# Performance work log

Hardware: AMD Instinct MI355X
Metric: run time of the kernel (lower is better)

The kernel has to match this reference:

```python
import jax, jax.numpy as jnp
import numpy as np

NUM_LANDMARKS = 256
PINV_ITERS = 6


def iterative_inv(K):
    # Newton-Schulz iterative pseudo-inverse (Nystromformer), K: [B, m, m]
    I = jnp.eye(K.shape[-1], dtype=K.dtype)
    V = K.swapaxes(-1, -2) / (jnp.max(jnp.sum(K, axis=-2)) * jnp.max(jnp.sum(K, axis=-1)))
    for _ in range(PINV_ITERS):
        KV = K @ V
        V = 0.25 * V @ (13.0 * I - KV @ (15.0 * I - KV @ (7.0 * I - KV)))
    return V


def nystrom_attention_matrix(q, k, m):
    # q, k: [B, N, d] -> approximate softmax(q k^T / sqrt(d)) of shape [B, N, N]
    B, N, d = q.shape
    scale = 1.0 / jnp.sqrt(jnp.asarray(d, q.dtype))
    L = N // m
    q_l = q.reshape(B, m, L, d).mean(axis=2)  # landmark queries [B, m, d]
    k_l = k.reshape(B, m, L, d).mean(axis=2)  # landmark keys    [B, m, d]
    k1 = jax.nn.softmax(jnp.einsum('bnd,bmd->bnm', q, k_l) * scale, axis=-1)   # [B, N, m]
    k2 = jax.nn.softmax(jnp.einsum('bld,bmd->blm', q_l, k_l) * scale, axis=-1) # [B, m, m]
    k3 = jax.nn.softmax(jnp.einsum('bmd,bnd->bmn', q_l, k) * scale, axis=-1)   # [B, m, N]
    return (k1 @ iterative_inv(k2)) @ k3  # [B, N, N]


def setup_inputs() -> dict:
    key = jax.random.key(0)
    ks = jax.random.split(key, 8)
    B, C, T, W, H = 2, 64, 4, 32, 32
    d = C // 8
    scale = 0.05  # keep q.k scores in a sane softmax range
    return {
        'x': jax.random.normal(ks[0], (B, C, T, W, H), dtype=jnp.float32),
        'wq': jax.random.normal(ks[1], (d, C), dtype=jnp.float32) * scale,
        'bq': jax.random.normal(ks[2], (d,), dtype=jnp.float32) * scale,
        'wk': jax.random.normal(ks[3], (d, C), dtype=jnp.float32) * scale,
        'bk': jax.random.normal(ks[4], (d,), dtype=jnp.float32) * scale,
        'wv': jax.random.normal(ks[5], (C, C), dtype=jnp.float32) * scale,
        'bv': jax.random.normal(ks[6], (C,), dtype=jnp.float32) * scale,
        'gamma': jax.random.normal(ks[7], (1,), dtype=jnp.float32),
    }


def reference(x, wq, bq, wk, bk, wv, bv, gamma):
    B, C, T, W, H = x.shape
    N = T * W * H
    xf = x.reshape(B, C, N)
    # 1x1x1 Conv3d == per-token linear over channels
    q = jnp.einsum('oc,bcn->bno', wq, xf) + bq            # [B, N, C//8]
    k = jnp.einsum('oc,bcn->bno', wk, xf) + bk            # [B, N, C//8]
    v = jnp.einsum('oc,bcn->bon', wv, xf) + bv[None, :, None]  # [B, C, N]
    attn = nystrom_attention_matrix(q, k, NUM_LANDMARKS)  # [B, N, N]
    # out = bmm(value, attn^T): out[b,c,i] = sum_j v[b,c,j] * attn[b,i,j]
    out = jnp.einsum('bcj,bij->bci', v, attn).reshape(B, C, T, W, H)
    out = gamma[0] * out + x
    return out, attn
```

## Files before the change

### kernel.cpp

```cpp
#include <hip/hip_runtime.h>
#include <hip/hip_bf16.h>
#include <math.h>

#define NB 2
#define NC 64
#define ND 8
#define NN 4096
#define NM 256
#define NL 16
#define SCALE 0.35355339059327373f
#define A_ROOT 4.1303956f
#define B_COEF (-2.8696044f)
#define C_COEF 3.1474086f

typedef __attribute__((ext_vector_type(4))) float f32x4;
typedef __attribute__((ext_vector_type(8))) short bf16x8;

__device__ inline ushort f2bf(float f) {
  __hip_bfloat16 h = __float2bfloat16(f);
  return *reinterpret_cast<ushort*>(&h);
}
__device__ inline float bf2f(ushort u) {
  return __uint_as_float(((unsigned int)u) << 16);
}

__device__ inline void gl_lds16(const void* g, void* l) {
  __builtin_amdgcn_global_load_lds(
      (const __attribute__((address_space(1))) unsigned int*)g,
      (__attribute__((address_space(3))) unsigned int*)l, 16, 0, 0);
}

__global__ __launch_bounds__(256) void qkv2_kernel(
    const float* __restrict__ x,
    const float* __restrict__ wq, const float* __restrict__ bq,
    const float* __restrict__ wk, const float* __restrict__ bk,
    const float* __restrict__ wv, const float* __restrict__ bv,
    float* __restrict__ q, float* __restrict__ k, float* __restrict__ v) {
  __shared__ float ws[NC];
  int o = blockIdx.x;
  int b = blockIdx.z;
  int n0 = blockIdx.y * 1024;
  int t = threadIdx.x;
  const float* wrow;
  float bias;
  if (o < ND)            { wrow = wq + (size_t)o * NC;            bias = bq[o]; }
  else if (o < 2 * ND)   { wrow = wk + (size_t)(o - ND) * NC;     bias = bk[o - ND]; }
  else                   { wrow = wv + (size_t)(o - 2 * ND) * NC; bias = bv[o - 2 * ND]; }
  if (t < NC) ws[t] = wrow[t];
  __syncthreads();
  int n = n0 + t * 4;
  float4 acc = {bias, bias, bias, bias};
  #pragma unroll
  for (int c = 0; c < NC; ++c) {
    float wc = ws[c];
    float4 xv = *(const float4*)(x + ((size_t)b * NC + c) * NN + n);
    acc.x += wc * xv.x; acc.y += wc * xv.y; acc.z += wc * xv.z; acc.w += wc * xv.w;
  }
  if (o < ND) {
    float* qp = q + ((size_t)b * NN + n) * ND + o;
    qp[0] = acc.x; qp[8] = acc.y; qp[16] = acc.z; qp[24] = acc.w;
  } else if (o < 2 * ND) {
    float* kp = k + ((size_t)b * NN + n) * ND + (o - ND);
    kp[0] = acc.x; kp[8] = acc.y; kp[16] = acc.z; kp[24] = acc.w;
  } else {
    *(float4*)(v + ((size_t)b * NC + (o - 2 * ND)) * NN + n) = acc;
  }
}

__global__ void landmark_kernel(const float* __restrict__ q, const float* __restrict__ k,
                                float* __restrict__ ql, float* __restrict__ kl) {
  int idx = blockIdx.x * 256 + threadIdx.x;
  int b = idx / (NM * ND), r = idx % (NM * ND), i = r / ND, o = r % ND;
  float sq = 0.f, sk = 0.f;
  for (int l = 0; l < NL; ++l) {
    size_t base = ((size_t)b * NN + i * NL + l) * ND + o;
    sq += q[base]; sk += k[base];
  }
  ql[idx] = sq * (1.0f / NL);
  kl[idx] = sk * (1.0f / NL);
}

__global__ __launch_bounds__(256) void scores_softmax_m_bf16(
    const float* __restrict__ Q, int R, const float* __restrict__ KL,
    ushort* __restrict__ out) {
  __shared__ float skl[NM][9];
  int b = blockIdx.y;
  int t = threadIdx.x;
  for (int i = t; i < NM * ND; i += 256) skl[i >> 3][i & 7] = KL[(size_t)b * NM * ND + i];
  __syncthreads();
  int wave = t >> 6, lane = t & 63;
  int r = blockIdx.x * 4 + wave;
  const float* qrow = Q + ((size_t)b * R + r) * ND;
  float qr[ND];
  #pragma unroll
  for (int dd = 0; dd < ND; ++dd) qr[dd] = qrow[dd];
  float sc[4];
  float lmax = -1e30f;
  #pragma unroll
  for (int s = 0; s < 4; ++s) {
    int j = lane + 64 * s;
    float a = 0.f;
    #pragma unroll
    for (int dd = 0; dd < ND; ++dd) a += qr[dd] * skl[j][dd];
    sc[s] = a * SCALE;
    lmax = fmaxf(lmax, sc[s]);
  }
  for (int off = 32; off; off >>= 1) lmax = fmaxf(lmax, __shfl_xor(lmax, off));
  float lsum = 0.f;
  #pragma unroll
  for (int s = 0; s < 4; ++s) { sc[s] = expf(sc[s] - lmax); lsum += sc[s]; }
  for (int off = 32; off; off >>= 1) lsum += __shfl_xor(lsum, off);
  float inv = 1.0f / lsum;
  #pragma unroll
  for (int s = 0; s < 4; ++s)
    out[((size_t)b * R + r) * NM + lane + 64 * s] = f2bf(sc[s] * inv);
}

__global__ __launch_bounds__(256) void scores_softmax_m_f32(
    const float* __restrict__ Q, int R, const float* __restrict__ KL,
    float* __restrict__ out) {
  __shared__ float skl[NM][9];
  int b = blockIdx.y;
  int t = threadIdx.x;
  for (int i = t; i < NM * ND; i += 256) skl[i >> 3][i & 7] = KL[(size_t)b * NM * ND + i];
  __syncthreads();
  int wave = t >> 6, lane = t & 63;
  int r = blockIdx.x * 4 + wave;
  const float* qrow = Q + ((size_t)b * R + r) * ND;
  float qr[ND];
  #pragma unroll
  for (int dd = 0; dd < ND; ++dd) qr[dd] = qrow[dd];
  float sc[4];
  float lmax = -1e30f;
  #pragma unroll
  for (int s = 0; s < 4; ++s) {
    int j = lane + 64 * s;
    float a = 0.f;
    #pragma unroll
    for (int dd = 0; dd < ND; ++dd) a += qr[dd] * skl[j][dd];
    sc[s] = a * SCALE;
    lmax = fmaxf(lmax, sc[s]);
  }
  for (int off = 32; off; off >>= 1) lmax = fmaxf(lmax, __shfl_xor(lmax, off));
  float lsum = 0.f;
  #pragma unroll
  for (int s = 0; s < 4; ++s) { sc[s] = expf(sc[s] - lmax); lsum += sc[s]; }
  for (int off = 32; off; off >>= 1) lsum += __shfl_xor(lsum, off);
  float inv = 1.0f / lsum;
  #pragma unroll
  for (int s = 0; s < 4; ++s) out[((size_t)b * R + r) * NM + lane + 64 * s] = sc[s] * inv;
}

__global__ __launch_bounds__(256) void scores_softmax_n(
    const float* __restrict__ QL, const float* __restrict__ Kt,
    float* __restrict__ out) {
  __shared__ float wred[4], wsum[4];
  int b = blockIdx.y, i = blockIdx.x;
  int t = threadIdx.x;
  float qr[ND];
  #pragma unroll
  for (int dd = 0; dd < ND; ++dd) qr[dd] = QL[((size_t)b * NM + i) * ND + dd];
  float sc[16];
  float lmax = -1e30f;
  #pragma unroll
  for (int s = 0; s < 16; ++s) {
    int n = t + 256 * s;
    const float* kp = Kt + ((size_t)b * NN + n) * ND;
    float a = 0.f;
    #pragma unroll
    for (int dd = 0; dd < ND; ++dd) a += qr[dd] * kp[dd];
    sc[s] = a * SCALE;
    lmax = fmaxf(lmax, sc[s]);
  }
  for (int off = 32; off; off >>= 1) lmax = fmaxf(lmax, __shfl_xor(lmax, off));
  if ((t & 63) == 0) wred[t >> 6] = lmax;
  __syncthreads();
  lmax = fmaxf(fmaxf(wred[0], wred[1]), fmaxf(wred[2], wred[3]));
  float lsum = 0.f;
  #pragma unroll
  for (int s = 0; s < 16; ++s) { sc[s] = expf(sc[s] - lmax); lsum += sc[s]; }
  for (int off = 32; off; off >>= 1) lsum += __shfl_xor(lsum, off);
  if ((t & 63) == 0) wsum[t >> 6] = lsum;
  __syncthreads();
  lsum = wsum[0] + wsum[1] + wsum[2] + wsum[3];
  float inv = 1.0f / lsum;
  #pragma unroll
  for (int s = 0; s < 16; ++s) out[((size_t)b * NM + i) * NN + t + 256 * s] = sc[s] * inv;
}

__global__ __launch_bounds__(256) void denom_kernel(const float* __restrict__ k2,
                                                    float* __restrict__ denw) {
  __shared__ float red[256];
  int b = blockIdx.x;
  int t = threadIdx.x;
  float cs = 0.f;
  for (int i = 0; i < NM; ++i) cs += k2[((size_t)b * NM + i) * NM + t];
  red[t] = cs;
  __syncthreads();
  for (int off = 128; off; off >>= 1) {
    if (t < off) red[t] = fmaxf(red[t], red[t + off]);
    __syncthreads();
  }
  if (t == 0) denw[b] = red[0];
}

__global__ void vinit_kernel(const float* __restrict__ k2, const float* __restrict__ denw,
                             float* __restrict__ V) {
  int idx = blockIdx.x * 256 + threadIdx.x;
  int b = idx / (NM * NM), r = idx % (NM * NM), i = r / NM, j = r % NM;
  float dval = 1.0f / fmaxf(denw[0], denw[1]);
  V[idx] = k2[((size_t)b * NM + j) * NM + i] * dval;
}

#define NS_SMEM 70144

__device__ __forceinline__ void pad_work(
    int p, const float* __restrict__ k3, ushort* __restrict__ k3t,
    const float* __restrict__ vw, float* __restrict__ kvw, char* smem, int t) {
  if (p < 2048) {
    typedef float TRow[33];
    TRow* tile = (TRow*)smem;
    int n0 = (p & 127) * 32, m0 = ((p >> 7) & 7) * 32, b = p >> 10;
    int rr = t >> 3, c4 = (t & 7) * 4;
    float4 v = *(const float4*)(k3 + ((size_t)b * NM + m0 + rr) * NN + n0 + c4);
    tile[c4][rr] = v.x; tile[c4 + 1][rr] = v.y; tile[c4 + 2][rr] = v.z; tile[c4 + 3][rr] = v.w;
    __syncthreads();
    ushort4 u;
    u.x = f2bf(tile[rr][c4]);     u.y = f2bf(tile[rr][c4 + 1]);
    u.z = f2bf(tile[rr][c4 + 2]); u.w = f2bf(tile[rr][c4 + 3]);
    *(ushort4*)(k3t + ((size_t)b * NN + n0 + rr) * NM + m0 + c4) = u;
  } else {
    typedef float KVRow[33];
    KVRow* Ks = (KVRow*)smem;
    KVRow* Vs = (KVRow*)(smem + 64 * 33 * 4);
    int p2 = p - 2048;
    int bp = (p2 & 3) * 64;
    int jsl = (p2 >> 2) & 31;
    int b = p2 >> 7;
    int j0base = jsl * (NN / 32);
    int tx = t & 15, ty = t >> 4;
    int lrow = t >> 2, ljc = (t & 3) * 8;
    float acc[4][4] = {};
    for (int j0 = j0base; j0 < j0base + NN / 32; j0 += 32) {
      float4 a0 = *(const float4*)(k3 + ((size_t)b * NM + bp + lrow) * NN + j0 + ljc);
      float4 a1 = *(const float4*)(k3 + ((size_t)b * NM + bp + lrow) * NN + j0 + ljc + 4);
      float4 v0 = *(const float4*)(vw + ((size_t)b * NC + lrow) * NN + j0 + ljc);
      float4 v1 = *(const float4*)(vw + ((size_t)b * NC + lrow) * NN + j0 + ljc + 4);
      Ks[lrow][ljc + 0] = a0.x; Ks[lrow][ljc + 1] = a0.y; Ks[lrow][ljc + 2] = a0.z; Ks[lrow][ljc + 3] = a0.w;
      Ks[lrow][ljc + 4] = a1.x; Ks[lrow][ljc + 5] = a1.y; Ks[lrow][ljc + 6] = a1.z; Ks[lrow][ljc + 7] = a1.w;
      Vs[lrow][ljc + 0] = v0.x; Vs[lrow][ljc + 1] = v0.y; Vs[lrow][ljc + 2] = v0.z; Vs[lrow][ljc + 3] = v0.w;
      Vs[lrow][ljc + 4] = v1.x; Vs[lrow][ljc + 5] = v1.y; Vs[lrow][ljc + 6] = v1.z; Vs[lrow][ljc + 7] = v1.w;
      __syncthreads();
      #pragma unroll
      for (int kk = 0; kk < 32; ++kk) {
        float av_[4], bv_[4];
        #pragma unroll
        for (int i = 0; i < 4; ++i) av_[i] = Ks[(ty << 2) + i][kk];
        #pragma unroll
        for (int j = 0; j < 4; ++j) bv_[j] = Vs[(tx << 2) + j][kk];
        #pragma unroll
        for (int i = 0; i < 4; ++i)
          #pragma unroll
          for (int j = 0; j < 4; ++j) acc[i][j] += av_[i] * bv_[j];
      }
      __syncthreads();
    }
    #pragma unroll
    for (int i = 0; i < 4; ++i)
      #pragma unroll
      for (int j = 0; j < 4; ++j)
        atomicAdd(&kvw[((size_t)b * NM + bp + (ty << 2) + i) * NC + (tx << 2) + j], acc[i][j]);
  }
}

__device__ __forceinline__ void ns_tile(
    const float* __restrict__ A, const float* __restrict__ B,
    const float* __restrict__ B2, float* __restrict__ O,
    float s_a, float s_ab, size_t bo, int bi, int bj, char* smem, int t) {
  typedef float ARow[260];
  typedef float BRow[36];
  ARow* As = (ARow*)smem;
  BRow* Bs = (BRow*)(smem + 33280);
  #pragma unroll
  for (int q = 0; q < 8; ++q) {
    int s = q * 256 + t;
    int ar = s >> 6, ac = (s & 63) * 4;
    *(float4*)&As[ar][ac] = *(const float4*)(A + bo + (size_t)(bi + ar) * NM + ac);
    int bk = s >> 3, bc = (s & 7) * 4;
    if (B2 == nullptr) {
      *(float4*)&Bs[bk][bc] = *(const float4*)(B + bo + (size_t)bk * NM + bj + bc);
    } else {
      float4 v = *(const float4*)(B + bo + (size_t)bk * NM + bj + bc);
      float4 z = *(const float4*)(B2 + bo + (size_t)bk * NM + bj + bc);
      float4 rr;
      rr.x = v.x + B_COEF * z.x; rr.y = v.y + B_COEF * z.y;
      rr.z = v.z + B_COEF * z.z; rr.w = v.w + B_COEF * z.w;
      int d = bk - bj - bc;
      if (d >= 0 && d < 4) ((float*)&rr)[d] += C_COEF;
      *(float4*)&Bs[bk][bc] = rr;
    }
  }
  __syncthreads();
  int tx = t & 15, ty = t >> 4;
  float acc[2][2] = {};
  #pragma unroll 8
  for (int kk = 0; kk < NM; ++kk) {
    float a0 = As[ty * 2][kk], a1 = As[ty * 2 + 1][kk];
    float b0 = Bs[kk][tx * 2], b1 = Bs[kk][tx * 2 + 1];
    acc[0][0] += a0 * b0; acc[0][1] += a0 * b1;
    acc[1][0] += a1 * b0; acc[1][1] += a1 * b1;
  }
  #pragma unroll
  for (int i = 0; i < 2; ++i)
    #pragma unroll
    for (int j = 0; j < 2; ++j) {
      size_t o = bo + (size_t)(bi + ty * 2 + i) * NM + bj + tx * 2 + j;
      float r = s_ab * acc[i][j];
      if (s_a != 0.0f) r += s_a * A[o];
      O[o] = r;
    }
}

__global__ __launch_bounds__(256) void ns_z_kernel(
    const float* __restrict__ k2, const float* __restrict__ V, float* __restrict__ Z,
    const float* __restrict__ k3, ushort* __restrict__ k3t,
    const float* __restrict__ vw, float* __restrict__ kvw, int padBase) {
  __shared__ char smem[NS_SMEM];
  int blk = blockIdx.x, t = threadIdx.x;
  if (blk < NB * 64) {
    int b = blk >> 6, tile = blk & 63;
    int bi = (tile >> 3) * 32, bj = (tile & 7) * 32;
    ns_tile(k2, V, nullptr, Z, 0.f, 1.f, (size_t)b * NM * NM, bi, bj, smem, t);
  } else {
    pad_work(padBase + blk - NB * 64, k3, k3t, vw, kvw, smem, t);
  }
}

__global__ __launch_bounds__(256) void ns_uz2_kernel(
    const float* __restrict__ V, const float* __restrict__ Z,
    float* __restrict__ U, float* __restrict__ Z2,
    const float* __restrict__ k3, ushort* __restrict__ k3t,
    const float* __restrict__ vw, float* __restrict__ kvw, int padBase) {
  __shared__ char smem[NS_SMEM];
  int blk = blockIdx.x, t = threadIdx.x;
  if (blk < NB * 64) {
    int b = blk >> 6, tile = blk & 63;
    int bi = (tile >> 3) * 32, bj = (tile & 7) * 32;
    ns_tile(V, Z, nullptr, U, -A_ROOT, 1.f, (size_t)b * NM * NM, bi, bj, smem, t);
  } else if (blk < 2 * NB * 64) {
    int r = blk - NB * 64;
    int b = r >> 6, tile = r & 63;
    int bi = (tile >> 3) * 32, bj = (tile & 7) * 32;
    ns_tile(Z, Z, nullptr, Z2, 0.f, 1.f, (size_t)b * NM * NM, bi, bj, smem, t);
  } else {
    pad_work(padBase + blk - 2 * NB * 64, k3, k3t, vw, kvw, smem, t);
  }
}

__global__ __launch_bounds__(256) void ns_v_kernel(
    const float* __restrict__ U, const float* __restrict__ Z2,
    const float* __restrict__ Z, float* __restrict__ Vout,
    const float* __restrict__ k3, ushort* __restrict__ k3t,
    const float* __restrict__ vw, float* __restrict__ kvw, int padBase) {
  __shared__ char smem[NS_SMEM];
  int blk = blockIdx.x, t = threadIdx.x;
  if (blk < NB * 64) {
    int b = blk >> 6, tile = blk & 63;
    int bi = (tile >> 3) * 32, bj = (tile & 7) * 32;
    ns_tile(U, Z2, Z, Vout, 0.f, -0.25f, (size_t)b * NM * NM, bi, bj, smem, t);
  } else {
    pad_work(padBase + blk - NB * 64, k3, k3t, vw, kvw, smem, t);
  }
}

__global__ __launch_bounds__(256) void cvt_vinv_kernel(const float* __restrict__ Va,
                                                       ushort* __restrict__ Vt) {
  int b = blockIdx.z;
  int n0 = blockIdx.x * 32, m0 = blockIdx.y * 32;
  __shared__ float tile[32][33];
  int t = threadIdx.x;
  int r = t >> 3, c4 = (t & 7) * 4;
  float4 v = *(const float4*)(Va + ((size_t)b * NM + m0 + r) * NM + n0 + c4);
  tile[c4][r] = v.x; tile[c4 + 1][r] = v.y; tile[c4 + 2][r] = v.z; tile[c4 + 3][r] = v.w;
  __syncthreads();
  ushort4 u;
  u.x = f2bf(tile[r][c4]);     u.y = f2bf(tile[r][c4 + 1]);
  u.z = f2bf(tile[r][c4 + 2]); u.w = f2bf(tile[r][c4 + 3]);
  *(ushort4*)(Vt + ((size_t)b * NM + n0 + r) * NM + m0 + c4) = u;
}

__global__ __launch_bounds__(256) void gemm_a_mfma(
    const ushort* __restrict__ k1bf, const ushort* __restrict__ Vt,
    ushort* __restrict__ Abf) {
  int b = blockIdx.z;
  int bi = blockIdx.y * 128, bj = blockIdx.x * 128;
  __shared__ ushort As[128 * 64];
  __shared__ ushort Bs[128 * 64];
  int t = threadIdx.x;
  int wave = t >> 6, lane = t & 63;
  int wr = wave >> 1, wc = wave & 1;
  const ushort* Ab = k1bf + (size_t)b * NN * NM;
  const ushort* Bb = Vt + (size_t)b * NM * NM;
  f32x4 acc[4][4] = {};
  for (int k0 = 0; k0 < NM; k0 += 64) {
    #pragma unroll
    for (int q = 0; q < 4; ++q) {
      int s = q * 256 + t;
      int r = s >> 3, c = s & 7;
      int cs = (c ^ (r & 7)) << 3;
      gl_lds16(Ab + (size_t)(bi + r) * NM + k0 + cs, As + (size_t)s * 8);
      gl_lds16(Bb + (size_t)(bj + r) * NM + k0 + cs, Bs + (size_t)s * 8);
    }
    __syncthreads();
    #pragma unroll
    for (int kk = 0; kk < 2; ++kk) {
      int koff = kk * 64 + (lane >> 4) * 16;
      bf16x8 af[4], bfv[4];
      #pragma unroll
      for (int mi = 0; mi < 4; ++mi) {
        int row = wr * 64 + mi * 16 + (lane & 15);
        af[mi] = *(const bf16x8*)((const char*)As + row * 128 + (koff ^ ((row & 7) << 4)));
      }
      #pragma unroll
      for (int nj = 0; nj < 4; ++nj) {
        int row = wc * 64 + nj * 16 + (lane & 15);
        bfv[nj] = *(const bf16x8*)((const char*)Bs + row * 128 + (koff ^ ((row & 7) << 4)));
      }
      #pragma unroll
      for (int mi = 0; mi < 4; ++mi)
        #pragma unroll
        for (int nj = 0; nj < 4; ++nj)
          acc[mi][nj] = __builtin_amdgcn_mfma_f32_16x16x32_bf16(af[mi], bfv[nj], acc[mi][nj], 0, 0, 0);
    }
    __syncthreads();
  }
  int col = lane & 15, rbase = (lane >> 4) * 4;
  #pragma unroll
  for (int mi = 0; mi < 4; ++mi)
    #pragma unroll
    for (int nj = 0; nj < 4; ++nj)
      #pragma unroll
      for (int r = 0; r < 4; ++r)
        Abf[((size_t)b * NN + bi + wr * 64 + mi * 16 + rbase + r) * NM
            + bj + wc * 64 + nj * 16 + col] = f2bf(acc[mi][nj][r]);
}

__global__ __launch_bounds__(256) void gemm_attn_mfma(
    const ushort* __restrict__ Abf, const ushort* __restrict__ K3T,
    float* __restrict__ attn) {
  int lin = blockIdx.z * 1024 + blockIdx.y * 32 + blockIdx.x;
  int swz = (lin & 7) * 256 + (lin >> 3);
  int b = swz >> 10;
  int rem = swz & 1023;
  int bi = (rem >> 5) * 128, bj = (rem & 31) * 128;
  __shared__ ushort As[128 * 64];
  __shared__ ushort Bs[128 * 64];
  int t = threadIdx.x;
  int wave = t >> 6, lane = t & 63;
  int wr = wave >> 1, wc = wave & 1;
  const ushort* Ab = Abf + (size_t)b * NN * NM;
  const ushort* Bb = K3T + (size_t)b * NN * NM;
  f32x4 acc[4][4] = {};
  for (int k0 = 0; k0 < NM; k0 += 64) {
    #pragma unroll
    for (int q = 0; q < 4; ++q) {
      int s = q * 256 + t;
      int r = s >> 3, c = s & 7;
      int cs = (c ^ (r & 7)) << 3;
      gl_lds16(Ab + (size_t)(bi + r) * NM + k0 + cs, As + (size_t)s * 8);
      gl_lds16(Bb + (size_t)(bj + r) * NM + k0 + cs, Bs + (size_t)s * 8);
    }
    __syncthreads();
    #pragma unroll
    for (int kk = 0; kk < 2; ++kk) {
      int koff = kk * 64 + (lane >> 4) * 16;
      bf16x8 af[4], bfv[4];
      #pragma unroll
      for (int mi = 0; mi < 4; ++mi) {
        int row = wr * 64 + mi * 16 + (lane & 15);
        af[mi] = *(const bf16x8*)((const char*)As + row * 128 + (koff ^ ((row & 7) << 4)));
      }
      #pragma unroll
      for (int nj = 0; nj < 4; ++nj) {
        int row = wc * 64 + nj * 16 + (lane & 15);
        bfv[nj] = *(const bf16x8*)((const char*)Bs + row * 128 + (koff ^ ((row & 7) << 4)));
      }
      #pragma unroll
      for (int mi = 0; mi < 4; ++mi)
        #pragma unroll
        for (int nj = 0; nj < 4; ++nj)
          acc[mi][nj] = __builtin_amdgcn_mfma_f32_16x16x32_bf16(af[mi], bfv[nj], acc[mi][nj], 0, 0, 0);
    }
    __syncthreads();
  }
  int col = lane & 15, rbase = (lane >> 4) * 4;
  #pragma unroll
  for (int mi = 0; mi < 4; ++mi)
    #pragma unroll
    for (int nj = 0; nj < 4; ++nj)
      #pragma unroll
      for (int r = 0; r < 4; ++r)
        attn[((size_t)b * NN + bi + wr * 64 + mi * 16 + rbase + r) * NN
             + bj + wc * 64 + nj * 16 + col] = acc[mi][nj][r];
  }

__global__ __launch_bounds__(256) void out_kernel(
    const ushort* __restrict__ Abf, const float* __restrict__ kvm,
    const float* __restrict__ x, const float* __restrict__ gamma,
    float* __restrict__ outp) {
  __shared__ float As[32 * 256];
  int blk = blockIdx.x;
  int b = blk / (NN / 32), n0 = (blk % (NN / 32)) * 32;
  int t = threadIdx.x;
  for (int it = 0; it < 32; ++it)
    As[it * 256 + (t ^ (it & 31))] = bf2f(Abf[((size_t)b * NN + n0 + it) * NM + t]);
  __syncthreads();
  int tn = t & 31, cg0 = (t >> 5) * 8;
  float g = gamma[0];
  float acc[8] = {};
  for (int p = 0; p < NM; ++p) {
    float a = As[tn * 256 + (p ^ (tn & 31))];
    float4 kv0 = *(const float4*)(kvm + ((size_t)b * NM + p) * NC + cg0);
    float4 kv1 = *(const float4*)(kvm + ((size_t)b * NM + p) * NC + cg0 + 4);
    acc[0] += a * kv0.x; acc[1] += a * kv0.y; acc[2] += a * kv0.z; acc[3] += a * kv0.w;
    acc[4] += a * kv1.x; acc[5] += a * kv1.y; acc[6] += a * kv1.z; acc[7] += a * kv1.w;
  }
  #pragma unroll
  for (int qd = 0; qd < 8; ++qd) {
    int c = cg0 + qd;
    size_t idx = ((size_t)b * NC + c) * NN + n0 + tn;
    outp[idx] = g * acc[qd] + x[idx];
  }
}

extern "C" void kernel_launch(void* const* d_in, const int* in_sizes, int n_in,
                              void* d_out, int out_size, void* d_ws, size_t ws_size,
                              hipStream_t stream) {
  const float* x     = (const float*)d_in[0];
  const float* wq    = (const float*)d_in[1];
  const float* bq    = (const float*)d_in[2];
  const float* wk    = (const float*)d_in[3];
  const float* bk    = (const float*)d_in[4];
  const float* wv    = (const float*)d_in[5];
  const float* bv    = (const float*)d_in[6];
  const float* gamma = (const float*)d_in[7];
  float* outp = (float*)d_out;
  float* attn = outp + (size_t)NB * NC * NN;
  float* w = (float*)d_ws;

  float* qw   = w;
  float* kw   = qw + 65536;
  float* vw   = kw + 65536;
  float* qlw  = vw + 524288;
  float* klw  = qlw + 4096;
  float* k1w  = klw + 4096;
  float* k2w  = k1w + 2097152;
  float* k3w  = k2w + 131072;
  float* Abuf = k3w + 2097152;
  float* Zb   = Abuf + 1048576;
  float* Z2b  = Zb + 131072;
  float* Ub   = Z2b + 131072;
  float* Va   = Ub + 131072;
  float* Vtw  = Va + 131072;
  float* kvw  = Vtw + 65536;
  float* denw = kvw + 32768;
  ushort* k1bf  = (ushort*)k1w;
  ushort* k3T   = (ushort*)k1w + 2097152;
  ushort* Abf   = (ushort*)Abuf;
  ushort* Vinvt = (ushort*)Vtw;

  hipMemsetAsync(kvw, 0, (size_t)NB * NM * NC * sizeof(float), stream);
  qkv2_kernel<<<dim3(80, NN / 1024, NB), dim3(256), 0, stream>>>(
      x, wq, bq, wk, bk, wv, bv, qw, kw, vw);
  landmark_kernel<<<dim3(NB * NM * ND / 256), dim3(256), 0, stream>>>(qw, kw, qlw, klw);
  scores_softmax_m_bf16<<<dim3(NN / 4, NB), dim3(256), 0, stream>>>(qw, NN, klw, k1bf);
  scores_softmax_m_f32<<<dim3(NM / 4, NB), dim3(256), 0, stream>>>(qlw, NM, klw, k2w);
  scores_softmax_n<<<dim3(NM, NB), dim3(256), 0, stream>>>(qlw, kw, k3w);
  denom_kernel<<<dim3(NB), dim3(256), 0, stream>>>(k2w, denw);
  vinit_kernel<<<dim3(NB * NM * NM / 256), dim3(256), 0, stream>>>(k2w, denw, Va);

  int padBase = 0;
  for (int it = 0; it < 6; ++it) {
    ns_z_kernel<<<dim3(NB * 64 + 128), dim3(256), 0, stream>>>(
        k2w, Va, Zb, k3w, k3T, vw, kvw, padBase);
    padBase += 128;
    ns_uz2_kernel<<<dim3(2 * NB * 64 + 128), dim3(256), 0, stream>>>(
        Va, Zb, Ub, Z2b, k3w, k3T, vw, kvw, padBase);
    padBase += 128;
    ns_v_kernel<<<dim3(NB * 64 + 128), dim3(256), 0, stream>>>(
        Ub, Z2b, Zb, Va, k3w, k3T, vw, kvw, padBase);
    padBase += 128;
  }

  cvt_vinv_kernel<<<dim3(NM / 32, NM / 32, NB), dim3(256), 0, stream>>>(Va, Vinvt);
  gemm_a_mfma<<<dim3(NM / 128, NN / 128, NB), dim3(256), 0, stream>>>(k1bf, Vinvt, Abf);
  gemm_attn_mfma<<<dim3(NN / 128, NN / 128, NB), dim3(256), 0, stream>>>(Abf, k3T, attn);
  out_kernel<<<dim3(NB * NN / 32), dim3(256), 0, stream>>>(Abf, kvw, x, gamma, outp);
}
```

Before: 312.4 us.

## Emit k3 directly as bf16 and read it via LDS transpose loads

The n-softmax kernel now writes k3 directly in bf16 in its natural [m, N] layout, which removes the separate fp32 k3 buffer and the transpose pass that was padded into the Newton-Schulz launches. The attention GEMM loads B tiles along rows of k3 and uses ds_read_b64_tr_b16 transpose reads to form MFMA operands. The k3·V product moves to a standalone kv_kernel launched after the attention GEMM. The NS kernels shrink back to their core tiles. The trade-off is that kv now runs serially instead of hiding in idle CUs during the NS iterations, and the kv product uses bf16 k3.

```diff
diff --git a/kernel.cpp b/kernel.cpp
--- a/kernel.cpp
+++ b/kernel.cpp
@@ -15,6 +15,7 @@
 
 typedef __attribute__((ext_vector_type(4))) float f32x4;
 typedef __attribute__((ext_vector_type(8))) short bf16x8;
+typedef __attribute__((ext_vector_type(4))) short bf16x4;
 
 __device__ inline ushort f2bf(float f) {
   __hip_bfloat16 h = __float2bfloat16(f);
@@ -28,6 +29,10 @@
   __builtin_amdgcn_global_load_lds(
       (const __attribute__((address_space(1))) unsigned int*)g,
       (__attribute__((address_space(3))) unsigned int*)l, 16, 0, 0);
+}
+
+__device__ inline unsigned lds_addr(const void* p) {
+  return (unsigned)(size_t)(__attribute__((address_space(3))) const void*)p;
 }
 
 __global__ __launch_bounds__(256) void qkv2_kernel(
@@ -153,7 +158,7 @@
 
 __global__ __launch_bounds__(256) void scores_softmax_n(
     const float* __restrict__ QL, const float* __restrict__ Kt,
-    float* __restrict__ out) {
+    ushort* __restrict__ out) {
   __shared__ float wred[4], wsum[4];
   int b = blockIdx.y, i = blockIdx.x;
   int t = threadIdx.x;
@@ -185,7 +190,8 @@
   lsum = wsum[0] + wsum[1] + wsum[2] + wsum[3];
   float inv = 1.0f / lsum;
   #pragma unroll
-  for (int s = 0; s < 16; ++s) out[((size_t)b * NM + i) * NN + t + 256 * s] = sc[s] * inv;
+  for (int s = 0; s < 16; ++s)
+    out[((size_t)b * NM + i) * NN + t + 256 * s] = f2bf(sc[s] * inv);
 }
 
 __global__ __launch_bounds__(256) void denom_kernel(const float* __restrict__ k2,
@@ -213,65 +219,6 @@
 }
 
 #define NS_SMEM 70144
-
-__device__ __forceinline__ void pad_work(
-    int p, const float* __restrict__ k3, ushort* __restrict__ k3t,
-    const float* __restrict__ vw, float* __restrict__ kvw, char* smem, int t) {
-  if (p < 2048) {
-    typedef float TRow[33];
-    TRow* tile = (TRow*)smem;
-    int n0 = (p & 127) * 32, m0 = ((p >> 7) & 7) * 32, b = p >> 10;
-    int rr = t >> 3, c4 = (t & 7) * 4;
-    float4 v = *(const float4*)(k3 + ((size_t)b * NM + m0 + rr) * NN + n0 + c4);
-    tile[c4][rr] = v.x; tile[c4 + 1][rr] = v.y; tile[c4 + 2][rr] = v.z; tile[c4 + 3][rr] = v.w;
-    __syncthreads();
-    ushort4 u;
-    u.x = f2bf(tile[rr][c4]);     u.y = f2bf(tile[rr][c4 + 1]);
-    u.z = f2bf(tile[rr][c4 + 2]); u.w = f2bf(tile[rr][c4 + 3]);
-    *(ushort4*)(k3t + ((size_t)b * NN + n0 + rr) * NM + m0 + c4) = u;
-  } else {
-    typedef float KVRow[33];
-    KVRow* Ks = (KVRow*)smem;
-    KVRow* Vs = (KVRow*)(smem + 64 * 33 * 4);
-    int p2 = p - 2048;
-    int bp = (p2 & 3) * 64;
-    int jsl = (p2 >> 2) & 31;
-    int b = p2 >> 7;
-    int j0base = jsl * (NN / 32);
-    int tx = t & 15, ty = t >> 4;
-    int lrow = t >> 2, ljc = (t & 3) * 8;
-    float acc[4][4] = {};
-    for (int j0 = j0base; j0 < j0base + NN / 32; j0 += 32) {
-      float4 a0 = *(const float4*)(k3 + ((size_t)b * NM + bp + lrow) * NN + j0 + ljc);
-      float4 a1 = *(const float4*)(k3 + ((size_t)b * NM + bp + lrow) * NN + j0 + ljc + 4);
-      float4 v0 = *(const float4*)(vw + ((size_t)b * NC + lrow) * NN + j0 + ljc);
-      float4 v1 = *(const float4*)(vw + ((size_t)b * NC + lrow) * NN + j0 + ljc + 4);
-      Ks[lrow][ljc + 0] = a0.x; Ks[lrow][ljc + 1] = a0.y; Ks[lrow][ljc + 2] = a0.z; Ks[lrow][ljc + 3] = a0.w;
-      Ks[lrow][ljc + 4] = a1.x; Ks[lrow][ljc + 5] = a1.y; Ks[lrow][ljc + 6] = a1.z; Ks[lrow][ljc + 7] = a1.w;
-      Vs[lrow][ljc + 0] = v0.x; Vs[lrow][ljc + 1] = v0.y; Vs[lrow][ljc + 2] = v0.z; Vs[lrow][ljc + 3] = v0.w;
-      Vs[lrow][ljc + 4] = v1.x; Vs[lrow][ljc + 5] = v1.y; Vs[lrow][ljc + 6] = v1.z; Vs[lrow][ljc + 7] = v1.w;
-      __syncthreads();
-      #pragma unroll
-      for (int kk = 0; kk < 32; ++kk) {
-        float av_[4], bv_[4];
-        #pragma unroll
-        for (int i = 0; i < 4; ++i) av_[i] = Ks[(ty << 2) + i][kk];
-        #pragma unroll
-        for (int j = 0; j < 4; ++j) bv_[j] = Vs[(tx << 2) + j][kk];
-        #pragma unroll
-        for (int i = 0; i < 4; ++i)
-          #pragma unroll
-          for (int j = 0; j < 4; ++j) acc[i][j] += av_[i] * bv_[j];
-      }
-      __syncthreads();
-    }
-    #pragma unroll
-    for (int i = 0; i < 4; ++i)
-      #pragma unroll
-      for (int j = 0; j < 4; ++j)
-        atomicAdd(&kvw[((size_t)b * NM + bp + (ty << 2) + i) * NC + (tx << 2) + j], acc[i][j]);
-  }
-}
 
 __device__ __forceinline__ void ns_tile(
     const float* __restrict__ A, const float* __restrict__ B,
@@ -322,55 +269,39 @@
 }
 
 __global__ __launch_bounds__(256) void ns_z_kernel(
-    const float* __restrict__ k2, const float* __restrict__ V, float* __restrict__ Z,
-    const float* __restrict__ k3, ushort* __restrict__ k3t,
-    const float* __restrict__ vw, float* __restrict__ kvw, int padBase) {
+    const float* __restrict__ k2, const float* __restrict__ V, float* __restrict__ Z) {
   __shared__ char smem[NS_SMEM];
   int blk = blockIdx.x, t = threadIdx.x;
-  if (blk < NB * 64) {
-    int b = blk >> 6, tile = blk & 63;
-    int bi = (tile >> 3) * 32, bj = (tile & 7) * 32;
-    ns_tile(k2, V, nullptr, Z, 0.f, 1.f, (size_t)b * NM * NM, bi, bj, smem, t);
-  } else {
-    pad_work(padBase + blk - NB * 64, k3, k3t, vw, kvw, smem, t);
-  }
+  int b = blk >> 6, tile = blk & 63;
+  int bi = (tile >> 3) * 32, bj = (tile & 7) * 32;
+  ns_tile(k2, V, nullptr, Z, 0.f, 1.f, (size_t)b * NM * NM, bi, bj, smem, t);
 }
 
 __global__ __launch_bounds__(256) void ns_uz2_kernel(
     const float* __restrict__ V, const float* __restrict__ Z,
-    float* __restrict__ U, float* __restrict__ Z2,
-    const float* __restrict__ k3, ushort* __restrict__ k3t,
-    const float* __restrict__ vw, float* __restrict__ kvw, int padBase) {
+    float* __restrict__ U, float* __restrict__ Z2) {
   __shared__ char smem[NS_SMEM];
   int blk = blockIdx.x, t = threadIdx.x;
   if (blk < NB * 64) {
     int b = blk >> 6, tile = blk & 63;
     int bi = (tile >> 3) * 32, bj = (tile & 7) * 32;
     ns_tile(V, Z, nullptr, U, -A_ROOT, 1.f, (size_t)b * NM * NM, bi, bj, smem, t);
-  } else if (blk < 2 * NB * 64) {
+  } else {
     int r = blk - NB * 64;
     int b = r >> 6, tile = r & 63;
     int bi = (tile >> 3) * 32, bj = (tile & 7) * 32;
     ns_tile(Z, Z, nullptr, Z2, 0.f, 1.f, (size_t)b * NM * NM, bi, bj, smem, t);
-  } else {
-    pad_work(padBase + blk - 2 * NB * 64, k3, k3t, vw, kvw, smem, t);
   }
 }
 
 __global__ __launch_bounds__(256) void ns_v_kernel(
     const float* __restrict__ U, const float* __restrict__ Z2,
-    const float* __restrict__ Z, float* __restrict__ Vout,
-    const float* __restrict__ k3, ushort* __restrict__ k3t,
-    const float* __restrict__ vw, float* __restrict__ kvw, int padBase) {
+    const float* __restrict__ Z, float* __restrict__ Vout) {
   __shared__ char smem[NS_SMEM];
   int blk = blockIdx.x, t = threadIdx.x;
-  if (blk < NB * 64) {
-    int b = blk >> 6, tile = blk & 63;
-    int bi = (tile >> 3) * 32, bj = (tile & 7) * 32;
-    ns_tile(U, Z2, Z, Vout, 0.f, -0.25f, (size_t)b * NM * NM, bi, bj, smem, t);
-  } else {
-    pad_work(padBase + blk - NB * 64, k3, k3t, vw, kvw, smem, t);
-  }
+  int b = blk >> 6, tile = blk & 63;
+  int bi = (tile >> 3) * 32, bj = (tile & 7) * 32;
+  ns_tile(U, Z2, Z, Vout, 0.f, -0.25f, (size_t)b * NM * NM, bi, bj, smem, t);
 }
 
 __global__ __launch_bounds__(256) void cvt_vinv_kernel(const float* __restrict__ Va,
@@ -446,7 +377,7 @@
 }
 
 __global__ __launch_bounds__(256) void gemm_attn_mfma(
-    const ushort* __restrict__ Abf, const ushort* __restrict__ K3T,
+    const ushort* __restrict__ Abf, const ushort* __restrict__ k3bf,
     float* __restrict__ attn) {
   int lin = blockIdx.z * 1024 + blockIdx.y * 32 + blockIdx.x;
   int swz = (lin & 7) * 256 + (lin >> 3);
@@ -454,13 +385,15 @@
   int rem = swz & 1023;
   int bi = (rem >> 5) * 128, bj = (rem & 31) * 128;
   __shared__ ushort As[128 * 64];
-  __shared__ ushort Bs[128 * 64];
+  __shared__ ushort Bs[8 * 64 * 16];
   int t = threadIdx.x;
   int wave = t >> 6, lane = t & 63;
   int wr = wave >> 1, wc = wave & 1;
   const ushort* Ab = Abf + (size_t)b * NN * NM;
-  const ushort* Bb = K3T + (size_t)b * NN * NM;
+  const ushort* Bb = k3bf + (size_t)b * NM * NN;
   f32x4 acc[4][4] = {};
+  unsigned bs_base = lds_addr(&Bs[0]);
+  unsigned trlane = (unsigned)((lane & 15) * 2 + (lane >> 4) * 256);
   for (int k0 = 0; k0 < NM; k0 += 64) {
     #pragma unroll
     for (int q = 0; q < 4; ++q) {
@@ -468,7 +401,9 @@
       int r = s >> 3, c = s & 7;
       int cs = (c ^ (r & 7)) << 3;
       gl_lds16(Ab + (size_t)(bi + r) * NM + k0 + cs, As + (size_t)s * 8);
-      gl_lds16(Bb + (size_t)(bj + r) * NM + k0 + cs, Bs + (size_t)s * 8);
+      int cq = s >> 7, kk2 = (s >> 1) & 63, hf = s & 1;
+      gl_lds16(Bb + (size_t)(k0 + kk2) * NN + bj + cq * 16 + hf * 8,
+               Bs + (size_t)s * 8);
     }
     __syncthreads();
     #pragma unroll
@@ -482,9 +417,16 @@
       }
       #pragma unroll
       for (int nj = 0; nj < 4; ++nj) {
-        int row = wc * 64 + nj * 16 + (lane & 15);
-        bfv[nj] = *(const bf16x8*)((const char*)Bs + row * 128 + (koff ^ ((row & 7) << 4)));
+        int cq = wc * 4 + nj;
+        unsigned a32 = bs_base + (unsigned)(cq * 2048 + kk * 1024) + trlane;
+        bf16x4 lo, hi;
+        asm volatile("ds_read_b64_tr_b16 %0, %2 offset:0\n\t"
+                     "ds_read_b64_tr_b16 %1, %2 offset:128"
+                     : "=&v"(lo), "=&v"(hi) : "v"(a32));
+        bfv[nj] = __builtin_shufflevector(lo, hi, 0, 1, 2, 3, 4, 5, 6, 7);
       }
+      asm volatile("s_waitcnt lgkmcnt(0)" ::: "memory");
+      __builtin_amdgcn_sched_barrier(0);
       #pragma unroll
       for (int mi = 0; mi < 4; ++mi)
         #pragma unroll
@@ -502,7 +444,46 @@
       for (int r = 0; r < 4; ++r)
         attn[((size_t)b * NN + bi + wr * 64 + mi * 16 + rbase + r) * NN
              + bj + wc * 64 + nj * 16 + col] = acc[mi][nj][r];
-  }
+}
+
+__global__ __launch_bounds__(256) void kv_kernel(
+    const ushort* __restrict__ K3, const float* __restrict__ Vv,
+    float* __restrict__ kvout) {
+  int b = blockIdx.z, bp = blockIdx.x * 64;
+  int j0base = blockIdx.y * (NN / 32);
+  __shared__ float Ks[64][33], Vs[64][33];
+  int t = threadIdx.x, tx = t & 15, ty = t >> 4;
+  int lrow = t >> 2, ljc = (t & 3) * 8;
+  float acc[4][4] = {};
+  for (int j0 = j0base; j0 < j0base + NN / 32; j0 += 32) {
+    bf16x8 a0 = *(const bf16x8*)(K3 + ((size_t)b * NM + bp + lrow) * NN + j0 + ljc);
+    float4 v0 = *(const float4*)(Vv + ((size_t)b * NC + lrow) * NN + j0 + ljc);
+    float4 v1 = *(const float4*)(Vv + ((size_t)b * NC + lrow) * NN + j0 + ljc + 4);
+    #pragma unroll
+    for (int e = 0; e < 8; ++e) Ks[lrow][ljc + e] = bf2f((ushort)a0[e]);
+    Vs[lrow][ljc + 0] = v0.x; Vs[lrow][ljc + 1] = v0.y; Vs[lrow][ljc + 2] = v0.z; Vs[lrow][ljc + 3] = v0.w;
+    Vs[lrow][ljc + 4] = v1.x; Vs[lrow][ljc + 5] = v1.y; Vs[lrow][ljc + 6] = v1.z; Vs[lrow][ljc + 7] = v1.w;
+    __syncthreads();
+    #pragma unroll
+    for (int kk = 0; kk < 32; ++kk) {
+      float av_[4], bv_[4];
+      #pragma unroll
+      for (int i = 0; i < 4; ++i) av_[i] = Ks[(ty << 2) + i][kk];
+      #pragma unroll
+      for (int j = 0; j < 4; ++j) bv_[j] = Vs[(tx << 2) + j][kk];
+      #pragma unroll
+      for (int i = 0; i < 4; ++i)
+        #pragma unroll
+        for (int j = 0; j < 4; ++j) acc[i][j] += av_[i] * bv_[j];
+    }
+    __syncthreads();
+  }
+  #pragma unroll
+  for (int i = 0; i < 4; ++i)
+    #pragma unroll
+    for (int j = 0; j < 4; ++j)
+      atomicAdd(&kvout[((size_t)b * NM + bp + (ty << 2) + i) * NC + (tx << 2) + j], acc[i][j]);
+}
 
 __global__ __launch_bounds__(256) void out_kernel(
     const ushort* __restrict__ Abf, const float* __restrict__ kvm,
@@ -555,8 +536,8 @@
   float* klw  = qlw + 4096;
   float* k1w  = klw + 4096;
   float* k2w  = k1w + 2097152;
-  float* k3w  = k2w + 131072;
-  float* Abuf = k3w + 2097152;
+  float* spare= k2w + 131072;
+  float* Abuf = spare + 2097152;
   float* Zb   = Abuf + 1048576;
   float* Z2b  = Zb + 131072;
   float* Ub   = Z2b + 131072;
@@ -565,7 +546,7 @@
   float* kvw  = Vtw + 65536;
   float* denw = kvw + 32768;
   ushort* k1bf  = (ushort*)k1w;
-  ushort* k3T   = (ushort*)k1w + 2097152;
+  ushort* k3bf  = (ushort*)k1w + 2097152;
   ushort* Abf   = (ushort*)Abuf;
   ushort* Vinvt = (ushort*)Vtw;
 
@@ -575,25 +556,19 @@
   landmark_kernel<<<dim3(NB * NM * ND / 256), dim3(256), 0, stream>>>(qw, kw, qlw, klw);
   scores_softmax_m_bf16<<<dim3(NN / 4, NB), dim3(256), 0, stream>>>(qw, NN, klw, k1bf);
   scores_softmax_m_f32<<<dim3(NM / 4, NB), dim3(256), 0, stream>>>(qlw, NM, klw, k2w);
-  scores_softmax_n<<<dim3(NM, NB), dim3(256), 0, stream>>>(qlw, kw, k3w);
+  scores_softmax_n<<<dim3(NM, NB), dim3(256), 0, stream>>>(qlw, kw, k3bf);
   denom_kernel<<<dim3(NB), dim3(256), 0, stream>>>(k2w, denw);
   vinit_kernel<<<dim3(NB * NM * NM / 256), dim3(256), 0, stream>>>(k2w, denw, Va);
 
-  int padBase = 0;
   for (int it = 0; it < 6; ++it) {
-    ns_z_kernel<<<dim3(NB * 64 + 128), dim3(256), 0, stream>>>(
-        k2w, Va, Zb, k3w, k3T, vw, kvw, padBase);
-    padBase += 128;
-    ns_uz2_kernel<<<dim3(2 * NB * 64 + 128), dim3(256), 0, stream>>>(
-        Va, Zb, Ub, Z2b, k3w, k3T, vw, kvw, padBase);
-    padBase += 128;
-    ns_v_kernel<<<dim3(NB * 64 + 128), dim3(256), 0, stream>>>(
-        Ub, Z2b, Zb, Va, k3w, k3T, vw, kvw, padBase);
-    padBase += 128;
+    ns_z_kernel<<<dim3(NB * 64), dim3(256), 0, stream>>>(k2w, Va, Zb);
+    ns_uz2_kernel<<<dim3(2 * NB * 64), dim3(256), 0, stream>>>(Va, Zb, Ub, Z2b);
+    ns_v_kernel<<<dim3(NB * 64), dim3(256), 0, stream>>>(Ub, Z2b, Zb, Va);
   }
 
   cvt_vinv_kernel<<<dim3(NM / 32, NM / 32, NB), dim3(256), 0, stream>>>(Va, Vinvt);
   gemm_a_mfma<<<dim3(NM / 128, NN / 128, NB), dim3(256), 0, stream>>>(k1bf, Vinvt, Abf);
-  gemm_attn_mfma<<<dim3(NN / 128, NN / 128, NB), dim3(256), 0, stream>>>(Abf, k3T, attn);
+  gemm_attn_mfma<<<dim3(NN / 128, NN / 128, NB), dim3(256), 0, stream>>>(Abf, k3bf, attn);
+  kv_kernel<<<dim3(NM / 64, 32, NB), dim3(256), 0, stream>>>(k3bf, vw, kvw);
   out_kernel<<<dim3(NB * NN / 32), dim3(256), 0, stream>>>(Abf, kvw, x, gamma, outp);
 }
```

New measurement: 317.9 us. Within noise of the previous version (+1.8%).
